# Performance work log

Measured on AMD Instinct MI355X. Metric: run time of the kernel, lower is better.

## Reference

```python
import jax, jax.numpy as jnp
import numpy as np

N_NODES = 50000
N_EDGES = 800000
D_IN = 128
D_HID = 128


def setup_inputs() -> dict:
    key = jax.random.key(0)
    ks = jax.random.split(key, 9)
    x = jax.random.normal(ks[0], (N_NODES, D_IN), dtype=jnp.float32)
    edge_index = jax.random.randint(ks[1], (2, N_EDGES), 0, N_NODES, dtype=jnp.int64)
    s = 1.0 / np.sqrt(D_IN)
    # SAGEConv params: lin_l acts on mean-aggregated neighbors (has bias),
    # lin_r acts on the root/self features (no bias). Stored as [in, out].
    Wl1 = jax.random.uniform(ks[2], (D_IN, D_HID), jnp.float32, -s, s)
    Wr1 = jax.random.uniform(ks[3], (D_IN, D_HID), jnp.float32, -s, s)
    b1 = jax.random.uniform(ks[4], (D_HID,), jnp.float32, -s, s)
    Wl2 = jax.random.uniform(ks[5], (D_HID, D_HID), jnp.float32, -s, s)
    Wr2 = jax.random.uniform(ks[6], (D_HID, D_HID), jnp.float32, -s, s)
    b2 = jax.random.uniform(ks[7], (D_HID,), jnp.float32, -s, s)
    return {"x": x, "edge_index": edge_index, "Wl1": Wl1, "Wr1": Wr1,
            "b1": b1, "Wl2": Wl2, "Wr2": Wr2, "b2": b2}


def _sage_conv(h, src, dst, n_nodes, Wl, Wr, b):
    # gather neighbor features, mean-aggregate at targets (PyG mean aggr)
    msg = h[src]  # [E, d]
    summed = jax.ops.segment_sum(msg, dst, num_segments=n_nodes)  # [N, d]
    cnt = jax.ops.segment_sum(jnp.ones((src.shape[0], 1), h.dtype), dst,
                              num_segments=n_nodes)  # [N, 1]
    agg = summed / jnp.maximum(cnt, 1.0)  # isolated nodes -> 0, matches scatter-mean
    return agg @ Wl + b + h @ Wr


def reference(x, edge_index, Wl1, Wr1, b1, Wl2, Wr2, b2):
    src = edge_index[0]  # source nodes j (messages flow j -> i)
    dst = edge_index[1]  # target nodes i
    n = x.shape[0]
    h = _sage_conv(x, src, dst, n, Wl1, Wr1, b1)
    h = jax.nn.relu(h)  # dropout is identity in eval mode
    out = _sage_conv(h, src, dst, n, Wl2, Wr2, b2)
    return out
```

## Files before the change

### kernel.cpp

```cpp
#include <hip/hip_runtime.h>
#include <hip/hip_bf16.h>

#define DD 128
#define BSH 8
#define CHUNK 4096

typedef __attribute__((ext_vector_type(8))) short short8v;
typedef __attribute__((ext_vector_type(4))) float f32x4;

static __device__ __forceinline__ ushort f2bf(float f) {
    __hip_bfloat16 b = __float2bfloat16(f);
    return *reinterpret_cast<ushort*>(&b);
}


__global__ __launch_bounds__(256) void k_prep(const int* __restrict__ ei,
                                              int* __restrict__ hist, int E, int NB, int nblk,
                                              const float* __restrict__ x,
                                              ushort* __restrict__ xbf, int n4, int castBlocks,
                                              const float* __restrict__ Wl1,
                                              const float* __restrict__ Wr1,
                                              ushort* __restrict__ Wt1,
                                              const float* __restrict__ Wl2,
                                              const float* __restrict__ Wr2,
                                              ushort* __restrict__ Wt2) {
    __shared__ int lh[256];
    int t = threadIdx.x;
    int b = blockIdx.x;

    if (b < nblk) {
        lh[t] = 0;
        __syncthreads();
        int e0 = b * CHUNK;
        int e1 = min(e0 + CHUNK, E);
        for (int e = e0 + t; e < e1; e += 256)
            atomicAdd(&lh[ei[E + e] >> BSH], 1);
        __syncthreads();
        if (t < NB) hist[b * NB + t] = lh[t];
        return;
    }
    b -= nblk;
    if (b < castBlocks) {
        int i = b * 256 + t;
        if (i < n4) {
            float4 v = reinterpret_cast<const float4*>(x)[i];
            ushort4 o;
            o.x = f2bf(v.x); o.y = f2bf(v.y); o.z = f2bf(v.z); o.w = f2bf(v.w);
            reinterpret_cast<ushort4*>(xbf)[i] = o;
        }
        return;
    }
    b -= castBlocks;
    {
        const float* Wl = (b < 128) ? Wl1 : Wl2;
        const float* Wr = (b < 128) ? Wr1 : Wr2;
        ushort* Wt = (b < 128) ? Wt1 : Wt2;
        int idx = (b & 127) * 256 + t;
        int nn = idx >> 8, k = idx & 255;
        float v = (k < 128) ? Wl[k * 128 + nn] : Wr[(k - 128) * 128 + nn];
        Wt[nn * 256 + k] = f2bf(v);
    }
}

__global__ __launch_bounds__(1024) void k_hscan(int* __restrict__ hist,
                                                int* __restrict__ bbase,
                                                int nblk, int NB, int E) {
    __shared__ int part[4][256];
    __shared__ int s[256];
    int t = threadIdx.x;
    int b = t & 255, g = t >> 8;
    int q = (nblk + 3) >> 2;
    int lo = g * q, hi = min(lo + q, nblk);
    int sum = 0;
    if (b < NB)
        for (int blk = lo; blk < hi; ++blk) sum += hist[blk * NB + b];
    part[g][b] = sum;
    __syncthreads();
    if (g == 0) s[b] = part[0][b] + part[1][b] + part[2][b] + part[3][b];
    __syncthreads();
    for (int off = 1; off < 256; off <<= 1) {
        int v = 0;
        if (g == 0 && b >= off) v = s[b - off];
        __syncthreads();
        if (g == 0) s[b] += v;
        __syncthreads();
    }
    int base = (b == 0) ? 0 : s[b - 1];
    if (g == 0 && b < NB) bbase[b] = base;
    if (t == 0) bbase[NB] = E;
    int run = base;
    for (int gg = 0; gg < g; ++gg) run += part[gg][b];
    if (b < NB)
        for (int blk = lo; blk < hi; ++blk) {
            int tmp = hist[blk * NB + b];
            hist[blk * NB + b] = run;
            run += tmp;
        }
}

__global__ __launch_bounds__(256) void k_scatter(const int* __restrict__ ei,
                                                 const int* __restrict__ hist,
                                                 uint* __restrict__ pairs, int E, int NB) {
    __shared__ int lofs[256];
    __shared__ int lh[256];
    int t = threadIdx.x;
    int blk = blockIdx.x;
    lh[t] = 0;
    if (t < NB) lofs[t] = hist[blk * NB + t];
    __syncthreads();
    int e0 = blk * CHUNK, e1 = min(e0 + CHUNK, E);
    for (int e = e0 + t; e < e1; e += 256) {
        int sN = ei[e];
        int d = ei[E + e];
        int b = d >> BSH;
        int lp = atomicAdd(&lh[b], 1);
        pairs[lofs[b] + lp] = ((uint)(d & 255) << 16) | (uint)sN;
    }
}

__global__ __launch_bounds__(256) void k_csr(const uint* __restrict__ pairs,
                                             const int* __restrict__ bbase,
                                             int* __restrict__ rowptr,
                                             ushort* __restrict__ eidx,
                                             int n, int E, int NB) {
    __shared__ int lc[256];
    __shared__ int cur[256];
    int t = threadIdx.x;
    int b = blockIdx.x;
    int node0 = b << BSH;
    lc[t] = 0;
    __syncthreads();
    int r0 = bbase[b], r1 = bbase[b + 1];
    for (int i = r0 + t; i < r1; i += 256)
        atomicAdd(&lc[pairs[i] >> 16], 1);
    __syncthreads();
    int c0 = lc[t];
#pragma unroll
    for (int off = 1; off < 256; off <<= 1) {
        int u = (t >= off) ? lc[t - off] : 0;
        __syncthreads();
        lc[t] += u;
        __syncthreads();
    }
    int rp = r0 + lc[t] - c0;
    int node = node0 + t;
    if (node < n) rowptr[node] = rp;
    if (b == NB - 1 && t == 0) rowptr[n] = E;
    cur[t] = rp;
    __syncthreads();
    for (int i = r0 + t; i < r1; i += 256) {
        uint pr = pairs[i];
        int p = atomicAdd(&cur[pr >> 16], 1);
        eidx[p] = (ushort)(pr & 0xFFFFu);
    }
}


#define ACC8(v)                                    \
    acc[0] += __uint_as_float((v).x << 16);        \
    acc[1] += __uint_as_float((v).x & 0xffff0000u);\
    acc[2] += __uint_as_float((v).y << 16);        \
    acc[3] += __uint_as_float((v).y & 0xffff0000u);\
    acc[4] += __uint_as_float((v).z << 16);        \
    acc[5] += __uint_as_float((v).z & 0xffff0000u);\
    acc[6] += __uint_as_float((v).w << 16);        \
    acc[7] += __uint_as_float((v).w & 0xffff0000u);

__global__ __launch_bounds__(256) void k_aggb(const ushort* __restrict__ hin,
                                              const int* __restrict__ rowptr,
                                              const ushort* __restrict__ eidx,
                                              ushort* __restrict__ aggout, int n) {
    int wave = (int)((blockIdx.x * (unsigned)blockDim.x + threadIdx.x) >> 6);
    int lane = threadIdx.x & 63;
    int grp = lane >> 4;
    int c16 = lane & 15;
    int node = wave * 4 + grp;
    if (node >= n) return;

    int beg = rowptr[node], end = rowptr[node + 1];
    const uint4* base = reinterpret_cast<const uint4*>(hin);

    float acc[8];
#pragma unroll
    for (int i = 0; i < 8; ++i) acc[i] = 0.f;

    for (int e = beg; e < end; e += 4) {
        int m = end - e;
        int i0 = eidx[e];
        int i1 = eidx[e + (m > 1 ? 1 : 0)];
        int i2 = eidx[e + (m > 2 ? 2 : 0)];
        int i3 = eidx[e + (m > 3 ? 3 : 0)];
        uint4 v0 = base[(size_t)i0 * 16 + c16];
        uint4 v1 = base[(size_t)i1 * 16 + c16];
        uint4 v2 = base[(size_t)i2 * 16 + c16];
        uint4 v3 = base[(size_t)i3 * 16 + c16];
        ACC8(v0);
        if (m > 1) { ACC8(v1); }
        if (m > 2) { ACC8(v2); }
        if (m > 3) { ACC8(v3); }
    }

    float inv = 1.0f / fmaxf((float)(end - beg), 1.0f);
    uint4 o;
    o.x = ((uint)f2bf(acc[1] * inv) << 16) | (uint)f2bf(acc[0] * inv);
    o.y = ((uint)f2bf(acc[3] * inv) << 16) | (uint)f2bf(acc[2] * inv);
    o.z = ((uint)f2bf(acc[5] * inv) << 16) | (uint)f2bf(acc[4] * inv);
    o.w = ((uint)f2bf(acc[7] * inv) << 16) | (uint)f2bf(acc[6] * inv);
    reinterpret_cast<uint4*>(aggout)[(size_t)node * 16 + c16] = o;
}


__global__ __launch_bounds__(512, 8) void k_mm(const ushort* __restrict__ Alow,
                                               const ushort* __restrict__ Ahigh,
                                               const ushort* __restrict__ Wt,
                                               const float* __restrict__ bias,
                                               void* __restrict__ outp,
                                               int n, int relu, int outBf16) {
    __shared__ ushort sA[32][256];

    int t = threadIdx.x;
    int row0 = blockIdx.x * 32;

#pragma unroll
    for (int i = t; i < 1024; i += 512) {
        int r = i >> 5, c = i & 31;
        int row = row0 + r;
        if (row >= n) row = n - 1;
        const ushort* src = (c < 16) ? (Alow + (size_t)row * DD + c * 8)
                                     : (Ahigh + (size_t)row * DD + (c - 16) * 8);
        uint4 v = *reinterpret_cast<const uint4*>(src);
        int cs = (c & 16) | ((c ^ r) & 15);
        *reinterpret_cast<uint4*>(&sA[r][cs * 8]) = v;
    }
    __syncthreads();

    int wv = t >> 6;
    int lane = t & 63;
    int lr = lane & 15;
    int lk = lane >> 4;

    short8v bf[8];
    const ushort* wbase = Wt + (size_t)(wv * 16 + lr) * 256 + lk * 8;
#pragma unroll
    for (int ks = 0; ks < 8; ++ks)
        bf[ks] = *reinterpret_cast<const short8v*>(wbase + ks * 32);

    int col = wv * 16 + lr;
    float bv = bias[col];

#pragma unroll
    for (int sub = 0; sub < 2; ++sub) {
        int m0 = sub * 16;
        int r = m0 + lr;
        f32x4 acc = (f32x4){0.f, 0.f, 0.f, 0.f};
#pragma unroll
        for (int ks = 0; ks < 8; ++ks) {
            int cc = ks * 4 + lk;
            int cs = (cc & 16) | ((cc ^ r) & 15);
            short8v af = *reinterpret_cast<const short8v*>(&sA[r][cs * 8]);
            acc = __builtin_amdgcn_mfma_f32_16x16x32_bf16(af, bf[ks], acc, 0, 0, 0);
        }
        int rowb = row0 + m0 + lk * 4;
#pragma unroll
        for (int q = 0; q < 4; ++q) {
            int row = rowb + q;
            if (row < n) {
                float v = acc[q] + bv;
                if (relu) v = fmaxf(v, 0.f);
                if (outBf16) {
                    reinterpret_cast<ushort*>(outp)[(size_t)row * DD + col] = f2bf(v);
                } else {
                    reinterpret_cast<float*>(outp)[(size_t)row * DD + col] = v;
                }
            }
        }
    }
}


extern "C" void kernel_launch(void* const* d_in, const int* in_sizes, int n_in,
                              void* d_out, int out_size, void* d_ws, size_t ws_size,
                              hipStream_t stream) {
    const float* x   = (const float*)d_in[0];
    const int*   ei  = (const int*)d_in[1];
    const float* Wl1 = (const float*)d_in[2];
    const float* Wr1 = (const float*)d_in[3];
    const float* b1  = (const float*)d_in[4];
    const float* Wl2 = (const float*)d_in[5];
    const float* Wr2 = (const float*)d_in[6];
    const float* b2  = (const float*)d_in[7];
    float* out = (float*)d_out;

    int n = in_sizes[0] / DD;
    int E = in_sizes[1] / 2;

    int NB   = (n + 255) >> 8;
    int nblk = (E + CHUNK - 1) / CHUNK;

    char* ws = (char*)d_ws;
    size_t off = 0;
    auto take = [&](size_t bytes) -> void* {
        void* p = ws + off;
        off = (off + bytes + 255) & ~(size_t)255;
        return p;
    };
    int* rowptr    = (int*)take(((size_t)n + 1) * 4);
    int* hist      = (int*)take((size_t)nblk * NB * 4);
    int* bbase     = (int*)take(((size_t)NB + 1) * 4);
    ushort* eidx   = (ushort*)take((size_t)E * 2 + 16);
    uint* pairs    = (uint*)take((size_t)E * 4);
    ushort* xbf    = (ushort*)take((size_t)n * DD * 2);
    ushort* hbf    = (ushort*)take((size_t)n * DD * 2);
    ushort* aggbf  = (ushort*)take((size_t)n * DD * 2);
    ushort* Wt1    = (ushort*)take((size_t)DD * 256 * 2);
    ushort* Wt2    = (ushort*)take((size_t)DD * 256 * 2);

    int n4 = n * DD / 4;
    int castBlocks = (n4 + 255) / 256;
    int prepBlocks = nblk + castBlocks + 256;

    k_prep<<<prepBlocks, 256, 0, stream>>>(ei, hist, E, NB, nblk,
                                           x, xbf, n4, castBlocks,
                                           Wl1, Wr1, Wt1, Wl2, Wr2, Wt2);
    k_hscan<<<1, 1024, 0, stream>>>(hist, bbase, nblk, NB, E);
    k_scatter<<<nblk, 256, 0, stream>>>(ei, hist, pairs, E, NB);
    k_csr<<<NB, 256, 0, stream>>>(pairs, bbase, rowptr, eidx, n, E, NB);

    int aggBlocks = (n + 15) / 16;
    int mmBlocks  = (n + 31) / 32;

    k_aggb<<<aggBlocks, 256, 0, stream>>>(xbf, rowptr, eidx, aggbf, n);
    k_mm<<<mmBlocks, 512, 0, stream>>>(aggbf, xbf, Wt1, b1, hbf, n, 1, 1);
    k_aggb<<<aggBlocks, 256, 0, stream>>>(hbf, rowptr, eidx, aggbf, n);
    k_mm<<<mmBlocks, 512, 0, stream>>>(aggbf, hbf, Wt2, b2, out, n, 0, 0);
}
```

Measured before the change: 159.9 us.

## Fuse neighbor mean-aggregation into the SAGE matmul kernel per 32-node tile

Each layer now runs one kernel: 512 threads gather and mean-aggregate the neighbors of 32 nodes straight into shared memory, load the root rows beside them, then run the MFMA matmul over both halves. This removes the write and re-read of the bf16 aggregate buffer and two launches. The gather loop also processes 8 edges at a time to keep more loads in flight. The trade-off is that the irregular gather and the matmul share a block, so load imbalance within a tile stalls its MFMA waves, and occupancy is capped at 6 blocks.

```diff
diff --git a/kernel.cpp b/kernel.cpp
--- a/kernel.cpp
+++ b/kernel.cpp
@@ -166,86 +166,92 @@
     acc[6] += __uint_as_float((v).w << 16);        \
     acc[7] += __uint_as_float((v).w & 0xffff0000u);
 
-__global__ __launch_bounds__(256) void k_aggb(const ushort* __restrict__ hin,
-                                              const int* __restrict__ rowptr,
-                                              const ushort* __restrict__ eidx,
-                                              ushort* __restrict__ aggout, int n) {
-    int wave = (int)((blockIdx.x * (unsigned)blockDim.x + threadIdx.x) >> 6);
-    int lane = threadIdx.x & 63;
+__global__ __launch_bounds__(512, 6) void k_fused(const ushort* __restrict__ hin,
+                                                  const int* __restrict__ rowptr,
+                                                  const ushort* __restrict__ eidx,
+                                                  const ushort* __restrict__ Wt,
+                                                  const float* __restrict__ bias,
+                                                  void* __restrict__ outp,
+                                                  int n, int relu, int outBf16) {
+    __shared__ ushort sagg[32][128];
+    __shared__ ushort sroot[32][128];
+
+    int t = threadIdx.x;
+    int node0 = blockIdx.x * 32;
+
+    {
+        int r = t >> 4, c = t & 15;
+        int row = node0 + r;
+        if (row >= n) row = n - 1;
+        uint4 v = *reinterpret_cast<const uint4*>(hin + (size_t)row * DD + c * 8);
+        int cs = c ^ (r & 15);
+        *reinterpret_cast<uint4*>(&sroot[r][cs * 8]) = v;
+    }
+
+    int wave = t >> 6;
+    int lane = t & 63;
     int grp = lane >> 4;
     int c16 = lane & 15;
-    int node = wave * 4 + grp;
-    if (node >= n) return;
-
-    int beg = rowptr[node], end = rowptr[node + 1];
-    const uint4* base = reinterpret_cast<const uint4*>(hin);
-
-    float acc[8];
-#pragma unroll
-    for (int i = 0; i < 8; ++i) acc[i] = 0.f;
-
-    for (int e = beg; e < end; e += 4) {
-        int m = end - e;
-        int i0 = eidx[e];
-        int i1 = eidx[e + (m > 1 ? 1 : 0)];
-        int i2 = eidx[e + (m > 2 ? 2 : 0)];
-        int i3 = eidx[e + (m > 3 ? 3 : 0)];
-        uint4 v0 = base[(size_t)i0 * 16 + c16];
-        uint4 v1 = base[(size_t)i1 * 16 + c16];
-        uint4 v2 = base[(size_t)i2 * 16 + c16];
-        uint4 v3 = base[(size_t)i3 * 16 + c16];
-        ACC8(v0);
-        if (m > 1) { ACC8(v1); }
-        if (m > 2) { ACC8(v2); }
-        if (m > 3) { ACC8(v3); }
-    }
-
-    float inv = 1.0f / fmaxf((float)(end - beg), 1.0f);
-    uint4 o;
-    o.x = ((uint)f2bf(acc[1] * inv) << 16) | (uint)f2bf(acc[0] * inv);
-    o.y = ((uint)f2bf(acc[3] * inv) << 16) | (uint)f2bf(acc[2] * inv);
-    o.z = ((uint)f2bf(acc[5] * inv) << 16) | (uint)f2bf(acc[4] * inv);
-    o.w = ((uint)f2bf(acc[7] * inv) << 16) | (uint)f2bf(acc[6] * inv);
-    reinterpret_cast<uint4*>(aggout)[(size_t)node * 16 + c16] = o;
-}
-
-
-__global__ __launch_bounds__(512, 8) void k_mm(const ushort* __restrict__ Alow,
-                                               const ushort* __restrict__ Ahigh,
-                                               const ushort* __restrict__ Wt,
-                                               const float* __restrict__ bias,
-                                               void* __restrict__ outp,
-                                               int n, int relu, int outBf16) {
-    __shared__ ushort sA[32][256];
-
-    int t = threadIdx.x;
-    int row0 = blockIdx.x * 32;
-
-#pragma unroll
-    for (int i = t; i < 1024; i += 512) {
-        int r = i >> 5, c = i & 31;
-        int row = row0 + r;
-        if (row >= n) row = n - 1;
-        const ushort* src = (c < 16) ? (Alow + (size_t)row * DD + c * 8)
-                                     : (Ahigh + (size_t)row * DD + (c - 16) * 8);
-        uint4 v = *reinterpret_cast<const uint4*>(src);
-        int cs = (c & 16) | ((c ^ r) & 15);
-        *reinterpret_cast<uint4*>(&sA[r][cs * 8]) = v;
-    }
-    __syncthreads();
-
-    int wv = t >> 6;
-    int lane = t & 63;
+    {
+        int node = node0 + wave * 4 + grp;
+        int beg = 0, end = 0;
+        if (node < n) { beg = rowptr[node]; end = rowptr[node + 1]; }
+        const uint4* base = reinterpret_cast<const uint4*>(hin);
+
+        float acc[8];
+#pragma unroll
+        for (int i = 0; i < 8; ++i) acc[i] = 0.f;
+
+        int e = beg;
+        for (; e + 8 <= end; e += 8) {
+            int id[8];
+            uint4 v[8];
+#pragma unroll
+            for (int j = 0; j < 8; ++j) id[j] = eidx[e + j];
+#pragma unroll
+            for (int j = 0; j < 8; ++j) v[j] = base[(size_t)id[j] * 16 + c16];
+#pragma unroll
+            for (int j = 0; j < 8; ++j) { ACC8(v[j]); }
+        }
+        for (; e < end; e += 4) {
+            int m = end - e;
+            int i0 = eidx[e];
+            int i1 = eidx[e + (m > 1 ? 1 : 0)];
+            int i2 = eidx[e + (m > 2 ? 2 : 0)];
+            int i3 = eidx[e + (m > 3 ? 3 : 0)];
+            uint4 v0 = base[(size_t)i0 * 16 + c16];
+            uint4 v1 = base[(size_t)i1 * 16 + c16];
+            uint4 v2 = base[(size_t)i2 * 16 + c16];
+            uint4 v3 = base[(size_t)i3 * 16 + c16];
+            ACC8(v0);
+            if (m > 1) { ACC8(v1); }
+            if (m > 2) { ACC8(v2); }
+            if (m > 3) { ACC8(v3); }
+        }
+
+        float inv = 1.0f / fmaxf((float)(end - beg), 1.0f);
+        uint4 o;
+        o.x = ((uint)f2bf(acc[1] * inv) << 16) | (uint)f2bf(acc[0] * inv);
+        o.y = ((uint)f2bf(acc[3] * inv) << 16) | (uint)f2bf(acc[2] * inv);
+        o.z = ((uint)f2bf(acc[5] * inv) << 16) | (uint)f2bf(acc[4] * inv);
+        o.w = ((uint)f2bf(acc[7] * inv) << 16) | (uint)f2bf(acc[6] * inv);
+        int r = wave * 4 + grp;
+        int cs = c16 ^ (r & 15);
+        *reinterpret_cast<uint4*>(&sagg[r][cs * 8]) = o;
+    }
+    __syncthreads();
+
     int lr = lane & 15;
     int lk = lane >> 4;
+    int nt = wave;
 
     short8v bf[8];
-    const ushort* wbase = Wt + (size_t)(wv * 16 + lr) * 256 + lk * 8;
+    const ushort* wbase = Wt + (size_t)(nt * 16 + lr) * 256 + lk * 8;
 #pragma unroll
     for (int ks = 0; ks < 8; ++ks)
         bf[ks] = *reinterpret_cast<const short8v*>(wbase + ks * 32);
 
-    int col = wv * 16 + lr;
+    int col = nt * 16 + lr;
     float bv = bias[col];
 
 #pragma unroll
@@ -254,13 +260,21 @@
         int r = m0 + lr;
         f32x4 acc = (f32x4){0.f, 0.f, 0.f, 0.f};
 #pragma unroll
-        for (int ks = 0; ks < 8; ++ks) {
+        for (int ks = 0; ks < 4; ++ks) {
             int cc = ks * 4 + lk;
-            int cs = (cc & 16) | ((cc ^ r) & 15);
-            short8v af = *reinterpret_cast<const short8v*>(&sA[r][cs * 8]);
+            int cs = cc ^ (r & 15);
+            short8v af = *reinterpret_cast<const short8v*>(&sagg[r][cs * 8]);
             acc = __builtin_amdgcn_mfma_f32_16x16x32_bf16(af, bf[ks], acc, 0, 0, 0);
         }
-        int rowb = row0 + m0 + lk * 4;
+#pragma unroll
+        for (int ks = 0; ks < 4; ++ks) {
+            int cc = ks * 4 + lk;
+            int cs = cc ^ (r & 15);
+            short8v af = *reinterpret_cast<const short8v*>(&sroot[r][cs * 8]);
+            acc = __builtin_amdgcn_mfma_f32_16x16x32_bf16(af, bf[ks + 4], acc, 0, 0, 0);
+        }
+
+        int rowb = node0 + m0 + lk * 4;
 #pragma unroll
         for (int q = 0; q < 4; ++q) {
             int row = rowb + q;
@@ -311,7 +325,6 @@
     uint* pairs    = (uint*)take((size_t)E * 4);
     ushort* xbf    = (ushort*)take((size_t)n * DD * 2);
     ushort* hbf    = (ushort*)take((size_t)n * DD * 2);
-    ushort* aggbf  = (ushort*)take((size_t)n * DD * 2);
     ushort* Wt1    = (ushort*)take((size_t)DD * 256 * 2);
     ushort* Wt2    = (ushort*)take((size_t)DD * 256 * 2);
 
@@ -326,11 +339,8 @@
     k_scatter<<<nblk, 256, 0, stream>>>(ei, hist, pairs, E, NB);
     k_csr<<<NB, 256, 0, stream>>>(pairs, bbase, rowptr, eidx, n, E, NB);
 
-    int aggBlocks = (n + 15) / 16;
-    int mmBlocks  = (n + 31) / 32;
-
-    k_aggb<<<aggBlocks, 256, 0, stream>>>(xbf, rowptr, eidx, aggbf, n);
-    k_mm<<<mmBlocks, 512, 0, stream>>>(aggbf, xbf, Wt1, b1, hbf, n, 1, 1);
-    k_aggb<<<aggBlocks, 256, 0, stream>>>(hbf, rowptr, eidx, aggbf, n);
-    k_mm<<<mmBlocks, 512, 0, stream>>>(aggbf, hbf, Wt2, b2, out, n, 0, 0);
-}
+    int fusedBlocks = (n + 31) / 32;
+
+    k_fused<<<fusedBlocks, 512, 0, stream>>>(xbf, rowptr, eidx, Wt1, b1, hbf, n, 1, 1);
+    k_fused<<<fusedBlocks, 512, 0, stream>>>(hbf, rowptr, eidx, Wt2, b2, out, n, 0, 0);
+}
```

Result: faster. 154.1 us, median of 2 (-3.6%).
